# Kernel tuning notes

Measured on AMD Instinct MI355X. Metric: run time of the kernel, lower is better.

The kernel has to match this reference:

```python
import jax, jax.numpy as jnp
import numpy as np
from jax import lax

DH = 256   # d_hidden
NL = 8     # number of wavenet cells
K = 3      # kernel_size
DIN = 16   # d_lag + d_cov
DOUT = 1
T, B = 1024, 64


def setup_inputs() -> dict:
    key = jax.random.key(0)
    ks = jax.random.split(key, 20)
    s = 0.05
    inp = {
        "X_emb": jax.random.randint(ks[0], (T, B, 1), 0, 10),
        "X_cov": jax.random.normal(ks[1], (T, B, 8), jnp.float32),
        "X_lag": jax.random.normal(ks[2], (T, B, 8), jnp.float32),
        "y": jax.random.normal(ks[3], (T, B, DOUT), jnp.float32),
        "domain": jax.random.uniform(ks[4], (B, 4), jnp.float32),
        "up_w": jax.random.normal(ks[5], (DIN, DH), jnp.float32) * s,
        "up_b": jnp.zeros((DH,), jnp.float32),
        "conv_dil_w": jax.random.normal(ks[6], (NL, 2 * DH, DH, K), jnp.float32) * s,
        "conv_dil_b": jnp.zeros((NL, 2 * DH), jnp.float32),
        "skip_w": jax.random.normal(ks[7], (NL, 2 * DH, DH), jnp.float32) * s,
        "skip_b": jnp.zeros((NL, 2 * DH), jnp.float32),
        "fc_w": jax.random.normal(ks[8], (DH, DH), jnp.float32) * s,
        "fc_b": jnp.zeros((DH,), jnp.float32),
        "loc_w": jax.random.normal(ks[9], (DH, DOUT), jnp.float32) * s,
        "loc_b": jnp.zeros((DOUT,), jnp.float32),
        "scale_w": jax.random.normal(ks[10], (DH, DOUT), jnp.float32) * s,
        "scale_b": jnp.zeros((DOUT,), jnp.float32),
        "d_outputseqlen": 24,
    }
    return inp


def _causal_conv(h, w, b, dil):
    # h: [B, C, T], w: [O, C, K] -> causal (left-padded) dilated conv
    pad = (w.shape[-1] - 1) * dil
    y = lax.conv_general_dilated(h, w, window_strides=(1,), padding=[(pad, 0)],
                                 rhs_dilation=(dil,),
                                 dimension_numbers=("NCH", "OIH", "NCH"))
    return y + b[None, :, None]


def _forward(X_cov, X_lag, y, up_w, up_b, conv_dil_w, conv_dil_b,
             skip_w, skip_b, fc_w, fc_b, loc_w, loc_b, scale_w, scale_b,
             d_outputseqlen):
    t = X_lag.shape[0]
    h = jnp.concatenate([X_lag, X_cov[:t]], axis=-1) @ up_w + up_b  # [T,B,DH]
    h = jnp.transpose(h, (1, 2, 0))  # [B, DH, T]
    skip = jnp.zeros_like(h)
    for i in range(NL):
        fg = _causal_conv(h, conv_dil_w[i], conv_dil_b[i], 2 ** i)  # [B,2DH,T]
        f, g = jnp.split(fg, 2, axis=1)
        gated = jnp.tanh(f) * jax.nn.sigmoid(g)  # [B,DH,T]
        hs = jnp.einsum("oc,bct->bot", skip_w[i], gated) + skip_b[i][None, :, None]
        h_next, skip_next = jnp.split(hs, 2, axis=1)
        h = h + h_next
        skip = skip + skip_next
    feat = jnp.transpose(skip, (2, 0, 1))  # [T,B,DH]
    ff = jax.nn.relu(feat @ fc_w + fc_b)
    tail = ff[-d_outputseqlen:]
    loc = tail @ loc_w + loc_b
    scale = jax.nn.softplus(tail @ scale_w + scale_b) + 1e-6
    yt = y[-d_outputseqlen:]
    log_prob = (-0.5 * ((yt - loc) / scale) ** 2
                - jnp.log(scale) - 0.5 * np.log(2.0 * np.pi))
    loss_y = -jnp.mean(log_prob)
    total_loss = loss_y  # loss_d forced to 0 in the original forward
    return total_loss, loss_y, loc, scale


def reference(X_emb, X_cov, X_lag, y, domain, up_w, up_b, conv_dil_w,
              conv_dil_b, skip_w, skip_b, fc_w, fc_b, loc_w, loc_b,
              scale_w, scale_b, d_outputseqlen):
    # X_emb and domain are unused with d_emb=[] and loss_d hard-set to 0.
    return _forward(X_cov, X_lag, y, up_w, up_b, conv_dil_w, conv_dil_b,
                    skip_w, skip_b, fc_w, fc_b, loc_w, loc_b,
                    scale_w, scale_b, d_outputseqlen)
```

## Files before the change

kernel.cpp:

```cpp
#include <hip/hip_runtime.h>
#include <math.h>

static constexpr int TT = 1024, BB = 64, DHID = 256, NLAY = 8, OSL = 24;
static constexpr int T0H = 192, THN = 832;
static constexpr int T0G = 256, TGN = 768;

typedef __attribute__((ext_vector_type(8))) short short8;
typedef __attribute__((ext_vector_type(4))) float f32x4;
typedef unsigned short u16;
typedef __attribute__((ext_vector_type(4))) unsigned short u16x4;
typedef unsigned int u32;

__device__ __forceinline__ u16 f2bf(float x) {
  u32 u = __float_as_uint(x);
  return (u16)((u + 0x7fffu + ((u >> 16) & 1u)) >> 16);
}
__device__ __forceinline__ float bf2f(u16 v) {
  return __uint_as_float((u32)v << 16);
}
__device__ __forceinline__ void gll16(const u16* g, u16* l) {
  __builtin_amdgcn_global_load_lds((const __attribute__((address_space(1))) void*)g,
                                   (__attribute__((address_space(3))) void*)l, 16, 0, 0);
}

__global__ __launch_bounds__(256) void wprep(
    const float* __restrict__ cw, const float* __restrict__ sw,
    u16* __restrict__ wP, u16* __restrict__ swH, u16* __restrict__ swG)
{
  const int stride = gridDim.x * 256;
  for (int i = blockIdx.x * 256 + threadIdx.x; i < NLAY * 3 * 8 * 2 * 4 * 2048; i += stride) {
    const int e = i & 7, row = (i >> 3) & 255;
    int q = i >> 11;
    const int p = q & 3; q >>= 2;
    const int cs = q & 1; q >>= 1;
    const int kc = q & 7; q >>= 3;
    const int tap = q % 3, l = q / 3;
    const int o = (row < 128) ? (cs * 128 + row) : (256 + cs * 128 + (row - 128));
    const int c = kc * 32 + p * 8 + e;
    wP[i] = f2bf(cw[((size_t)(l * 512 + o) * 256 + c) * 3 + tap]);
  }
  for (int i = blockIdx.x * 256 + threadIdx.x; i < NLAY * 8 * 4 * 2048; i += stride) {
    const int e = i & 7, o = (i >> 3) & 255, p = (i >> 11) & 3, kc = (i >> 13) & 7, l = i >> 16;
    const int c = kc * 32 + p * 8 + e;
    swH[i] = f2bf(sw[(size_t)(l * 512 + o) * 256 + c]);
    swG[i] = f2bf(sw[(size_t)(l * 512 + 256 + o) * 256 + c]);
  }
}

__global__ __launch_bounds__(256) void up_kernel(
    const float* __restrict__ xlag, const float* __restrict__ xcov,
    const float* __restrict__ upw, const float* __restrict__ upb,
    u16* __restrict__ hb0)
{
  const int b  = blockIdx.y;
  const int t0 = T0H + blockIdx.x * 16;
  __shared__ float xs[16][17];
  {
    const int tl = threadIdx.x >> 4;
    const int j  = threadIdx.x & 15;
    const size_t base = ((size_t)(t0 + tl) * BB + b) * 8;
    xs[tl][j] = (j < 8) ? xlag[base + j] : xcov[base + (j - 8)];
  }
  __syncthreads();
  const int c = threadIdx.x;
  float uw[16];
#pragma unroll
  for (int j = 0; j < 16; ++j) uw[j] = upw[j * DHID + c];
  const float bias = upb[c];
#pragma unroll
  for (int tl = 0; tl < 16; ++tl) {
    float acc = bias;
#pragma unroll
    for (int j = 0; j < 16; ++j) acc = fmaf(xs[tl][j], uw[j], acc);
    hb0[(((size_t)b * 32 + (c >> 3)) * THN + (t0 + tl - T0H)) * 8 + (c & 7)] = f2bf(acc);
  }
}

__global__ __launch_bounds__(1024) void conv_gate(
    const u16* __restrict__ hbin, const u16* __restrict__ wPl,
    const float* __restrict__ cb, u16* __restrict__ gbuf,
    u16* __restrict__ g15l, const int dil, const int tile0)
{
  __shared__ u16 AB[2][16384];
  const int tid = threadIdx.x, w = tid >> 6, lane = tid & 63;
  const int l16 = lane & 15, quad = lane >> 4;
  const int mw = w & 3, nw = w >> 2;
  const int tile = tile0 + (int)(blockIdx.x >> 4);
  const int b0 = (blockIdx.x & 15) * 4;
  const int cs = blockIdx.y;
  const int t0 = tile * 64;

  f32x4 acc[4][4];
  const f32x4 zero = {0.f, 0.f, 0.f, 0.f};
#pragma unroll
  for (int m = 0; m < 4; ++m)
#pragma unroll
    for (int j = 0; j < 4; ++j) acc[m][j] = zero;

  const int ctb = tid >> 8, pb = (tid >> 6) & 3, tlb = tid & 63;

  auto stage = [&](int buf, int tap, int kc) {
    gll16(wPl + (size_t)(((tap * 8 + kc) * 2 + cs)) * 8192 + tid * 8,
          &AB[buf][(tid & ~63) * 8]);
    const int sh = (2 - tap) * dil;
    gll16(hbin + (((size_t)(b0 + ctb) * 32 + kc * 4 + pb) * THN + (t0 - sh - T0H + tlb)) * 8,
          &AB[buf][8192 + (tid & ~63) * 8]);
  };

  stage(0, 0, 0);
  __syncthreads();
  for (int step = 0; step < 24; ++step) {
    const int ns = step + 1;
    if (ns < 24) stage(ns & 1, ns >> 3, ns & 7);
    const u16* A = AB[step & 1];
    const u16* B = AB[step & 1] + 8192;
    short8 bfr[4];
#pragma unroll
    for (int j = 0; j < 4; ++j)
      bfr[j] = *(const short8*)&B[(nw * 256 + quad * 64 + 16 * j + l16) * 8];
#pragma unroll
    for (int m = 0; m < 4; ++m) {
      const int rowbase = (m < 2) ? (mw * 32 + 16 * m) : (128 + mw * 32 + 16 * (m - 2));
      const short8 a = *(const short8*)&A[(quad * 256 + rowbase + l16) * 8];
#pragma unroll
      for (int j = 0; j < 4; ++j)
        acc[m][j] = __builtin_amdgcn_mfma_f32_16x16x32_bf16(a, bfr[j], acc[m][j], 0, 0, 0);
    }
    __syncthreads();
  }

  u16* gT = (u16*)AB;
#pragma unroll
  for (int m = 0; m < 2; ++m) {
    const int c4 = mw * 32 + 16 * m + quad * 4;
    const int cpl = c4 >> 3;
#pragma unroll
    for (int j = 0; j < 4; ++j) {
      const int tl = 16 * j + l16;
      u16x4 pk;
#pragma unroll
      for (int r = 0; r < 4; ++r) {
        const float f = acc[m][j][r]     + cb[cs * 128 + c4 + r];
        const float g = acc[m + 2][j][r] + cb[256 + cs * 128 + c4 + r];
        const float th = 2.f / (1.f + __expf(-2.f * f)) - 1.f;
        const float sg = 1.f / (1.f + __expf(-g));
        pk[r] = f2bf(th * sg);
      }
      *(u16x4*)&gT[((nw * 16 + cpl) * 64 + tl) * 8 + (quad & 1) * 4] = pk;
    }
  }
  __syncthreads();
#pragma unroll
  for (int k = 0; k < 4; ++k) {
    const int slot = k * 1024 + tid;
    const int ct = slot >> 10, cpl = (slot >> 6) & 15, tl = slot & 63;
    const short8 v = *(const short8*)&gT[slot * 8];
    const int b = b0 + ct, cpg = cs * 16 + cpl;
    *(short8*)&gbuf[(((size_t)b * 32 + cpg) * TGN + (t0 + tl - T0G)) * 8] = v;
    if (tile == 15)
      *(short8*)&g15l[(((size_t)b * 32 + cpg) * 64 + tl) * 8] = v;
  }
}

__global__ __launch_bounds__(1024) void skip_h(
    const u16* __restrict__ gbuf, const u16* __restrict__ swHl,
    const float* __restrict__ sb, const u16* __restrict__ hbin,
    u16* __restrict__ hbout, const int tile0)
{
  __shared__ u16 AB[2][16384];
  const int tid = threadIdx.x, w = tid >> 6, lane = tid & 63;
  const int l16 = lane & 15, quad = lane >> 4;
  const int mw = w & 3, nw = w >> 2;
  const int tile = tile0 + (int)(blockIdx.x >> 4);
  const int b0 = (blockIdx.x & 15) * 4;
  const int t0 = tile * 64;

  f32x4 acc[4][4];
  const f32x4 zero = {0.f, 0.f, 0.f, 0.f};
#pragma unroll
  for (int m = 0; m < 4; ++m)
#pragma unroll
    for (int j = 0; j < 4; ++j) acc[m][j] = zero;

  const int ctb = tid >> 8, pb = (tid >> 6) & 3, tlb = tid & 63;

  auto stage = [&](int buf, int kc) {
    gll16(swHl + (size_t)kc * 8192 + tid * 8, &AB[buf][(tid & ~63) * 8]);
    gll16(gbuf + (((size_t)(b0 + ctb) * 32 + kc * 4 + pb) * TGN + (t0 - T0G + tlb)) * 8,
          &AB[buf][8192 + (tid & ~63) * 8]);
  };

  stage(0, 0);
  __syncthreads();
  for (int step = 0; step < 8; ++step) {
    if (step + 1 < 8) stage((step + 1) & 1, step + 1);
    const u16* A = AB[step & 1];
    const u16* B = AB[step & 1] + 8192;
    short8 bfr[4];
#pragma unroll
    for (int j = 0; j < 4; ++j)
      bfr[j] = *(const short8*)&B[(nw * 256 + quad * 64 + 16 * j + l16) * 8];
#pragma unroll
    for (int m = 0; m < 4; ++m) {
      const short8 a = *(const short8*)&A[(quad * 256 + mw * 64 + 16 * m + l16) * 8];
#pragma unroll
      for (int j = 0; j < 4; ++j)
        acc[m][j] = __builtin_amdgcn_mfma_f32_16x16x32_bf16(a, bfr[j], acc[m][j], 0, 0, 0);
    }
    __syncthreads();
  }

  float* fT = (float*)AB;
  for (int ctr = 0; ctr < 4; ++ctr) {
    __syncthreads();
    if (nw == ctr) {
#pragma unroll
      for (int m = 0; m < 4; ++m) {
        const int c4 = mw * 64 + 16 * m + quad * 4;
#pragma unroll
        for (int j = 0; j < 4; ++j) {
          const int tl = 16 * j + l16;
          f32x4 v;
#pragma unroll
          for (int r = 0; r < 4; ++r) v[r] = acc[m][j][r] + sb[c4 + r];
          *(f32x4*)&fT[((c4 >> 3) * 64 + tl) * 8 + (quad & 1) * 4] = v;
        }
      }
    }
    __syncthreads();
    const int b = b0 + ctr;
#pragma unroll
    for (int k = 0; k < 2; ++k) {
      const int slot = k * 1024 + tid;
      const int cpl = slot >> 6, tl = slot & 63;
      const size_t idx = (((size_t)b * 32 + cpl) * THN + (t0 - T0H + tl)) * 8;
      const short8 hv = *(const short8*)&hbin[idx];
      short8 ov;
#pragma unroll
      for (int e = 0; e < 8; ++e)
        ov[e] = (short)f2bf(bf2f((u16)hv[e]) + fT[slot * 8 + e]);
      *(short8*)&hbout[idx] = ov;
    }
  }
}

__global__ __launch_bounds__(1024) void skip_g_final(
    const u16* __restrict__ g15, const u16* __restrict__ swG,
    float* __restrict__ skipf)
{
  __shared__ u16 AB[2][10240];
  const int tid = threadIdx.x, w = tid >> 6, lane = tid & 63;
  const int l16 = lane & 15, quad = lane >> 4;
  const int b = blockIdx.x;

  f32x4 acc[4];
  const f32x4 zero = {0.f, 0.f, 0.f, 0.f};
#pragma unroll
  for (int j = 0; j < 4; ++j) acc[j] = zero;

  auto stage = [&](int buf, int ks) {
    gll16(swG + (size_t)ks * 8192 + tid * 8, &AB[buf][(tid & ~63) * 8]);
    if (tid < 256) {
      const int p = tid >> 6, tl = tid & 63;
      const int l = ks >> 3, kc = ks & 7;
      gll16(g15 + ((((size_t)l * 64 + b) * 32 + kc * 4 + p) * 64 + tl) * 8,
            &AB[buf][8192 + (tid & ~63) * 8]);
    }
  };

  stage(0, 0);
  __syncthreads();
  for (int step = 0; step < 64; ++step) {
    if (step + 1 < 64) stage((step + 1) & 1, step + 1);
    const u16* A = AB[step & 1];
    const u16* B = AB[step & 1] + 8192;
    const short8 a = *(const short8*)&A[(quad * 256 + w * 16 + l16) * 8];
#pragma unroll
    for (int j = 0; j < 4; ++j) {
      const short8 bf = *(const short8*)&B[(quad * 64 + 16 * j + l16) * 8];
      acc[j] = __builtin_amdgcn_mfma_f32_16x16x32_bf16(a, bf, acc[j], 0, 0, 0);
    }
    __syncthreads();
  }
#pragma unroll
  for (int j = 0; j < 4; ++j)
#pragma unroll
    for (int r = 0; r < 4; ++r) {
      const int c = w * 16 + quad * 4 + r;
      skipf[((size_t)b * 256 + c) * 64 + 16 * j + l16] = acc[j][r];
    }
}

__global__ __launch_bounds__(256) void head_kernel(
    const float* __restrict__ skipf, const float* __restrict__ skip_b,
    const float* __restrict__ fcw, const float* __restrict__ fcb,
    const float* __restrict__ locw, const float* __restrict__ locb,
    const float* __restrict__ scw, const float* __restrict__ scb,
    float* __restrict__ out)
{
  const int tt = blockIdx.x;
  const int b  = blockIdx.y;
  const int tl = 40 + tt;
  const int c  = threadIdx.x;
  __shared__ float xs[DHID];
  float sbg = 0.f;
#pragma unroll
  for (int l = 0; l < NLAY; ++l) sbg += skip_b[l * 512 + 256 + c];
  xs[c] = skipf[((size_t)b * 256 + c) * 64 + tl] + sbg;
  __syncthreads();
  float acc = fcb[c];
#pragma unroll 8
  for (int j = 0; j < DHID; ++j) acc = fmaf(xs[j], fcw[j * DHID + c], acc);
  const float ff = fmaxf(acc, 0.f);
  float pl = ff * locw[c];
  float ps = ff * scw[c];
#pragma unroll
  for (int off = 32; off > 0; off >>= 1) {
    pl += __shfl_down(pl, off);
    ps += __shfl_down(ps, off);
  }
  __shared__ float rl[4], rs[4];
  const int wid = threadIdx.x >> 6, lane = threadIdx.x & 63;
  if (lane == 0) { rl[wid] = pl; rs[wid] = ps; }
  __syncthreads();
  if (threadIdx.x == 0) {
    const float loc = rl[0] + rl[1] + rl[2] + rl[3] + locb[0];
    const float x   = rs[0] + rs[1] + rs[2] + rs[3] + scb[0];
    const float sp  = (x > 0.f) ? (x + log1pf(expf(-x))) : log1pf(expf(x));
    out[2 + tt * BB + b]            = loc;
    out[2 + OSL * BB + tt * BB + b] = sp + 1e-6f;
  }
}

__global__ __launch_bounds__(256) void loss_kernel(
    const float* __restrict__ y, float* __restrict__ out)
{
  float s = 0.f;
  for (int i = threadIdx.x; i < OSL * BB; i += 256) {
    const int tt = i >> 6, b = i & 63;
    const float loc = out[2 + i];
    const float sc  = out[2 + OSL * BB + i];
    const float yt  = y[(size_t)(TT - OSL + tt) * BB + b];
    const float z   = (yt - loc) / sc;
    s += -0.5f * z * z - logf(sc) - 0.9189385332046727f;
  }
#pragma unroll
  for (int off = 32; off > 0; off >>= 1) s += __shfl_down(s, off);
  __shared__ float r[4];
  if ((threadIdx.x & 63) == 0) r[threadIdx.x >> 6] = s;
  __syncthreads();
  if (threadIdx.x == 0) {
    const float loss = -(r[0] + r[1] + r[2] + r[3]) / (float)(OSL * BB);
    out[0] = loss;
    out[1] = loss;
  }
}

extern "C" void kernel_launch(void* const* d_in, const int* in_sizes, int n_in,
                              void* d_out, int out_size, void* d_ws, size_t ws_size,
                              hipStream_t stream) {
  (void)in_sizes; (void)n_in; (void)out_size; (void)ws_size;
  const float* X_cov  = (const float*)d_in[1];
  const float* X_lag  = (const float*)d_in[2];
  const float* y      = (const float*)d_in[3];
  const float* up_w   = (const float*)d_in[5];
  const float* up_b   = (const float*)d_in[6];
  const float* conv_w = (const float*)d_in[7];
  const float* conv_b = (const float*)d_in[8];
  const float* skip_w = (const float*)d_in[9];
  const float* skip_b = (const float*)d_in[10];
  const float* fc_w   = (const float*)d_in[11];
  const float* fc_b   = (const float*)d_in[12];
  const float* loc_w  = (const float*)d_in[13];
  const float* loc_b  = (const float*)d_in[14];
  const float* sc_w   = (const float*)d_in[15];
  const float* sc_b   = (const float*)d_in[16];

  char* wsb = (char*)d_ws;
  u16*   hb0   = (u16*)(wsb + 0);
  u16*   hb1   = (u16*)(wsb + 27262976);
  u16*   gbuf  = (u16*)(wsb + 54525952);
  u16*   g15   = (u16*)(wsb + 79691776);
  u16*   wP    = (u16*)(wsb + 96468992);
  u16*   swH   = (u16*)(wsb + 102760448);
  u16*   swG   = (u16*)(wsb + 103809024);
  float* skipf = (float*)(wsb + 104857600);

  wprep<<<1024, 256, 0, stream>>>(conv_w, skip_w, wP, swH, swG);
  up_kernel<<<dim3(52, BB), 256, 0, stream>>>(X_lag, X_cov, up_w, up_b, hb0);

  static const int Ptab[NLAY] = {4, 5, 6, 7, 8, 9, 11, 15};
  u16* hin = hb0;
  u16* hout = hb1;
  for (int i = 0; i < NLAY; ++i) {
    const int ntiles = 16 - Ptab[i];
    conv_gate<<<dim3(ntiles * 16, 2), 1024, 0, stream>>>(
        hin, wP + (size_t)i * 393216, conv_b + i * 512, gbuf,
        g15 + (size_t)i * 1048576, 1 << i, Ptab[i]);
    skip_h<<<dim3(ntiles * 16), 1024, 0, stream>>>(
        gbuf, swH + (size_t)i * 65536, skip_b + i * 512, hin, hout, Ptab[i]);
    u16* tmp = hin; hin = hout; hout = tmp;
  }

  skip_g_final<<<dim3(64), 1024, 0, stream>>>(g15, swG, skipf);
  head_kernel<<<dim3(OSL, BB), 256, 0, stream>>>(
      skipf, skip_b, fc_w, fc_b, loc_w, loc_b, sc_w, sc_b, (float*)d_out);
  loss_kernel<<<1, 256, 0, stream>>>(y, (float*)d_out);
}
```

Measured before the change: 665.8 us.

## Halve block sizes, split output channels finer, and parallelize final skip GEMM by layer

conv_gate now uses 512-thread blocks covering 64 output channels each, with four channel splits instead of two, and the weight prepack layout changes to match. skip_h uses 512-thread blocks over two batch entries each, doubling the grid. The serial 64-step final skip GEMM becomes a per-layer grid over only the needed 32 time steps, and the head sums the per-layer partials. The aim is more blocks and better occupancy on a machine with many CUs, at the cost of more redundant activation loads per block and extra partial-sum traffic.

```diff
diff --git a/kernel.cpp b/kernel.cpp
--- a/kernel.cpp
+++ b/kernel.cpp
@@ -28,14 +28,12 @@
     u16* __restrict__ wP, u16* __restrict__ swH, u16* __restrict__ swG)
 {
   const int stride = gridDim.x * 256;
-  for (int i = blockIdx.x * 256 + threadIdx.x; i < NLAY * 3 * 8 * 2 * 4 * 2048; i += stride) {
-    const int e = i & 7, row = (i >> 3) & 255;
-    int q = i >> 11;
-    const int p = q & 3; q >>= 2;
-    const int cs = q & 1; q >>= 1;
-    const int kc = q & 7; q >>= 3;
+  for (int i = blockIdx.x * 256 + threadIdx.x; i < NLAY * 3 * 8 * 4 * 4 * 128 * 8; i += stride) {
+    const int e = i & 7, row = (i >> 3) & 127;
+    const int p = (i >> 10) & 3, cs = (i >> 12) & 3, kc = (i >> 14) & 7;
+    const int q = i >> 17;
     const int tap = q % 3, l = q / 3;
-    const int o = (row < 128) ? (cs * 128 + row) : (256 + cs * 128 + (row - 128));
+    const int o = (row < 64) ? (cs * 64 + row) : (256 + cs * 64 + (row - 64));
     const int c = kc * 32 + p * 8 + e;
     wP[i] = f2bf(cw[((size_t)(l * 512 + o) * 256 + c) * 3 + tap]);
   }
@@ -76,15 +74,15 @@
   }
 }
 
-__global__ __launch_bounds__(1024) void conv_gate(
+__global__ __launch_bounds__(512, 6) void conv_gate(
     const u16* __restrict__ hbin, const u16* __restrict__ wPl,
     const float* __restrict__ cb, u16* __restrict__ gbuf,
     u16* __restrict__ g15l, const int dil, const int tile0)
 {
-  __shared__ u16 AB[2][16384];
+  __shared__ u16 AB[2][12288];
   const int tid = threadIdx.x, w = tid >> 6, lane = tid & 63;
   const int l16 = lane & 15, quad = lane >> 4;
-  const int mw = w & 3, nw = w >> 2;
+  const int mw = w & 1, nw = w >> 1;
   const int tile = tile0 + (int)(blockIdx.x >> 4);
   const int b0 = (blockIdx.x & 15) * 4;
   const int cs = blockIdx.y;
@@ -97,14 +95,17 @@
 #pragma unroll
     for (int j = 0; j < 4; ++j) acc[m][j] = zero;
 
-  const int ctb = tid >> 8, pb = (tid >> 6) & 3, tlb = tid & 63;
-
   auto stage = [&](int buf, int tap, int kc) {
-    gll16(wPl + (size_t)(((tap * 8 + kc) * 2 + cs)) * 8192 + tid * 8,
+    gll16(wPl + ((size_t)((tap * 8 + kc) * 4 + cs)) * 4096 + tid * 8,
           &AB[buf][(tid & ~63) * 8]);
     const int sh = (2 - tap) * dil;
-    gll16(hbin + (((size_t)(b0 + ctb) * 32 + kc * 4 + pb) * THN + (t0 - sh - T0H + tlb)) * 8,
-          &AB[buf][8192 + (tid & ~63) * 8]);
+#pragma unroll
+    for (int q = 0; q < 2; ++q) {
+      const int s = q * 512 + tid;
+      const int ct = s >> 8, p = (s >> 6) & 3, tl = s & 63;
+      gll16(hbin + (((size_t)(b0 + ct) * 32 + kc * 4 + p) * THN + (t0 - sh - T0H + tl)) * 8,
+            &AB[buf][4096 + (s & ~63) * 8]);
+    }
   };
 
   stage(0, 0, 0);
@@ -113,15 +114,15 @@
     const int ns = step + 1;
     if (ns < 24) stage(ns & 1, ns >> 3, ns & 7);
     const u16* A = AB[step & 1];
-    const u16* B = AB[step & 1] + 8192;
+    const u16* B = AB[step & 1] + 4096;
     short8 bfr[4];
 #pragma unroll
     for (int j = 0; j < 4; ++j)
       bfr[j] = *(const short8*)&B[(nw * 256 + quad * 64 + 16 * j + l16) * 8];
 #pragma unroll
     for (int m = 0; m < 4; ++m) {
-      const int rowbase = (m < 2) ? (mw * 32 + 16 * m) : (128 + mw * 32 + 16 * (m - 2));
-      const short8 a = *(const short8*)&A[(quad * 256 + rowbase + l16) * 8];
+      const int row = (m < 2) ? (mw * 32 + 16 * m) : (64 + mw * 32 + 16 * (m - 2));
+      const short8 a = *(const short8*)&A[(quad * 128 + row + l16) * 8];
 #pragma unroll
       for (int j = 0; j < 4; ++j)
         acc[m][j] = __builtin_amdgcn_mfma_f32_16x16x32_bf16(a, bfr[j], acc[m][j], 0, 0, 0);
@@ -133,46 +134,45 @@
 #pragma unroll
   for (int m = 0; m < 2; ++m) {
     const int c4 = mw * 32 + 16 * m + quad * 4;
-    const int cpl = c4 >> 3;
 #pragma unroll
     for (int j = 0; j < 4; ++j) {
       const int tl = 16 * j + l16;
       u16x4 pk;
 #pragma unroll
       for (int r = 0; r < 4; ++r) {
-        const float f = acc[m][j][r]     + cb[cs * 128 + c4 + r];
-        const float g = acc[m + 2][j][r] + cb[256 + cs * 128 + c4 + r];
+        const float f = acc[m][j][r]     + cb[cs * 64 + c4 + r];
+        const float g = acc[m + 2][j][r] + cb[256 + cs * 64 + c4 + r];
         const float th = 2.f / (1.f + __expf(-2.f * f)) - 1.f;
         const float sg = 1.f / (1.f + __expf(-g));
         pk[r] = f2bf(th * sg);
       }
-      *(u16x4*)&gT[((nw * 16 + cpl) * 64 + tl) * 8 + (quad & 1) * 4] = pk;
+      *(u16x4*)&gT[((nw * 8 + (c4 >> 3)) * 64 + tl) * 8 + (c4 & 7)] = pk;
     }
   }
   __syncthreads();
 #pragma unroll
   for (int k = 0; k < 4; ++k) {
-    const int slot = k * 1024 + tid;
-    const int ct = slot >> 10, cpl = (slot >> 6) & 15, tl = slot & 63;
+    const int slot = k * 512 + tid;
+    const int ct = slot >> 9, cpl = (slot >> 6) & 7, tl = slot & 63;
     const short8 v = *(const short8*)&gT[slot * 8];
-    const int b = b0 + ct, cpg = cs * 16 + cpl;
+    const int b = b0 + ct, cpg = cs * 8 + cpl;
     *(short8*)&gbuf[(((size_t)b * 32 + cpg) * TGN + (t0 + tl - T0G)) * 8] = v;
     if (tile == 15)
       *(short8*)&g15l[(((size_t)b * 32 + cpg) * 64 + tl) * 8] = v;
   }
 }
 
-__global__ __launch_bounds__(1024) void skip_h(
+__global__ __launch_bounds__(512, 6) void skip_h(
     const u16* __restrict__ gbuf, const u16* __restrict__ swHl,
     const float* __restrict__ sb, const u16* __restrict__ hbin,
     u16* __restrict__ hbout, const int tile0)
 {
-  __shared__ u16 AB[2][16384];
+  __shared__ u16 AB[2][12288];
   const int tid = threadIdx.x, w = tid >> 6, lane = tid & 63;
   const int l16 = lane & 15, quad = lane >> 4;
   const int mw = w & 3, nw = w >> 2;
-  const int tile = tile0 + (int)(blockIdx.x >> 4);
-  const int b0 = (blockIdx.x & 15) * 4;
+  const int tile = tile0 + (int)(blockIdx.x >> 5);
+  const int b0 = (blockIdx.x & 31) * 2;
   const int t0 = tile * 64;
 
   f32x4 acc[4][4];
@@ -182,11 +182,14 @@
 #pragma unroll
     for (int j = 0; j < 4; ++j) acc[m][j] = zero;
 
-  const int ctb = tid >> 8, pb = (tid >> 6) & 3, tlb = tid & 63;
-
   auto stage = [&](int buf, int kc) {
-    gll16(swHl + (size_t)kc * 8192 + tid * 8, &AB[buf][(tid & ~63) * 8]);
-    gll16(gbuf + (((size_t)(b0 + ctb) * 32 + kc * 4 + pb) * TGN + (t0 - T0G + tlb)) * 8,
+#pragma unroll
+    for (int q = 0; q < 2; ++q) {
+      const int s = q * 512 + tid;
+      gll16(swHl + (size_t)kc * 8192 + s * 8, &AB[buf][(s & ~63) * 8]);
+    }
+    const int ct = tid >> 8, p = (tid >> 6) & 3, tl = tid & 63;
+    gll16(gbuf + (((size_t)(b0 + ct) * 32 + kc * 4 + p) * TGN + (t0 - T0G + tl)) * 8,
           &AB[buf][8192 + (tid & ~63) * 8]);
   };
 
@@ -211,88 +214,103 @@
   }
 
   float* fT = (float*)AB;
-  for (int ctr = 0; ctr < 4; ++ctr) {
-    __syncthreads();
-    if (nw == ctr) {
-#pragma unroll
-      for (int m = 0; m < 4; ++m) {
-        const int c4 = mw * 64 + 16 * m + quad * 4;
-#pragma unroll
-        for (int j = 0; j < 4; ++j) {
-          const int tl = 16 * j + l16;
-          f32x4 v;
-#pragma unroll
-          for (int r = 0; r < 4; ++r) v[r] = acc[m][j][r] + sb[c4 + r];
-          *(f32x4*)&fT[((c4 >> 3) * 64 + tl) * 8 + (quad & 1) * 4] = v;
+  for (int ctr = 0; ctr < 2; ++ctr) {
+    for (int hh = 0; hh < 2; ++hh) {
+      __syncthreads();
+      if (nw == ctr && (mw >> 1) == hh) {
+#pragma unroll
+        for (int m = 0; m < 4; ++m) {
+          const int c4 = mw * 64 + 16 * m + quad * 4;
+          const int rl = c4 & 127;
+#pragma unroll
+          for (int j = 0; j < 4; ++j) {
+            const int tl = 16 * j + l16;
+            f32x4 v;
+#pragma unroll
+            for (int r = 0; r < 4; ++r) v[r] = acc[m][j][r] + sb[c4 + r];
+            *(f32x4*)&fT[((rl >> 3) * 64 + tl) * 8 + (rl & 7)] = v;
+          }
         }
       }
-    }
-    __syncthreads();
-    const int b = b0 + ctr;
-#pragma unroll
-    for (int k = 0; k < 2; ++k) {
-      const int slot = k * 1024 + tid;
-      const int cpl = slot >> 6, tl = slot & 63;
-      const size_t idx = (((size_t)b * 32 + cpl) * THN + (t0 - T0H + tl)) * 8;
-      const short8 hv = *(const short8*)&hbin[idx];
-      short8 ov;
-#pragma unroll
-      for (int e = 0; e < 8; ++e)
-        ov[e] = (short)f2bf(bf2f((u16)hv[e]) + fT[slot * 8 + e]);
-      *(short8*)&hbout[idx] = ov;
-    }
-  }
-}
-
-__global__ __launch_bounds__(1024) void skip_g_final(
+      __syncthreads();
+      const int b = b0 + ctr;
+#pragma unroll
+      for (int k = 0; k < 2; ++k) {
+        const int slot = k * 512 + tid;
+        const int cpl = slot >> 6, tl = slot & 63;
+        const size_t idx = (((size_t)b * 32 + hh * 16 + cpl) * THN + (t0 - T0H + tl)) * 8;
+        const short8 hv = *(const short8*)&hbin[idx];
+        short8 ov;
+#pragma unroll
+        for (int e = 0; e < 8; ++e)
+          ov[e] = (short)f2bf(bf2f((u16)hv[e]) + fT[slot * 8 + e]);
+        *(short8*)&hbout[idx] = ov;
+      }
+    }
+  }
+}
+
+__global__ __launch_bounds__(512) void skip_g(
     const u16* __restrict__ g15, const u16* __restrict__ swG,
-    float* __restrict__ skipf)
-{
-  __shared__ u16 AB[2][10240];
+    float* __restrict__ gpart)
+{
+  __shared__ u16 AB[2][9216];
   const int tid = threadIdx.x, w = tid >> 6, lane = tid & 63;
   const int l16 = lane & 15, quad = lane >> 4;
-  const int b = blockIdx.x;
-
-  f32x4 acc[4];
+  const int b = blockIdx.x, l = blockIdx.y;
+
+  f32x4 acc[2][2];
   const f32x4 zero = {0.f, 0.f, 0.f, 0.f};
 #pragma unroll
-  for (int j = 0; j < 4; ++j) acc[j] = zero;
-
-  auto stage = [&](int buf, int ks) {
-    gll16(swG + (size_t)ks * 8192 + tid * 8, &AB[buf][(tid & ~63) * 8]);
-    if (tid < 256) {
-      const int p = tid >> 6, tl = tid & 63;
-      const int l = ks >> 3, kc = ks & 7;
-      gll16(g15 + ((((size_t)l * 64 + b) * 32 + kc * 4 + p) * 64 + tl) * 8,
+  for (int m = 0; m < 2; ++m)
+#pragma unroll
+    for (int j = 0; j < 2; ++j) acc[m][j] = zero;
+
+  auto stage = [&](int buf, int kc) {
+#pragma unroll
+    for (int q = 0; q < 2; ++q) {
+      const int s = q * 512 + tid;
+      gll16(swG + ((size_t)l * 8 + kc) * 8192 + s * 8, &AB[buf][(s & ~63) * 8]);
+    }
+    if (tid < 128) {
+      const int p = tid >> 5, tl = tid & 31;
+      gll16(g15 + ((((size_t)l * 64 + b) * 32 + kc * 4 + p) * 64 + 32 + tl) * 8,
             &AB[buf][8192 + (tid & ~63) * 8]);
     }
   };
 
   stage(0, 0);
   __syncthreads();
-  for (int step = 0; step < 64; ++step) {
-    if (step + 1 < 64) stage((step + 1) & 1, step + 1);
+  for (int step = 0; step < 8; ++step) {
+    if (step + 1 < 8) stage((step + 1) & 1, step + 1);
     const u16* A = AB[step & 1];
     const u16* B = AB[step & 1] + 8192;
-    const short8 a = *(const short8*)&A[(quad * 256 + w * 16 + l16) * 8];
-#pragma unroll
-    for (int j = 0; j < 4; ++j) {
-      const short8 bf = *(const short8*)&B[(quad * 64 + 16 * j + l16) * 8];
-      acc[j] = __builtin_amdgcn_mfma_f32_16x16x32_bf16(a, bf, acc[j], 0, 0, 0);
+    short8 bfr[2];
+#pragma unroll
+    for (int j = 0; j < 2; ++j)
+      bfr[j] = *(const short8*)&B[(quad * 32 + 16 * j + l16) * 8];
+#pragma unroll
+    for (int m = 0; m < 2; ++m) {
+      const short8 a = *(const short8*)&A[(quad * 256 + w * 32 + 16 * m + l16) * 8];
+#pragma unroll
+      for (int j = 0; j < 2; ++j)
+        acc[m][j] = __builtin_amdgcn_mfma_f32_16x16x32_bf16(a, bfr[j], acc[m][j], 0, 0, 0);
     }
     __syncthreads();
   }
 #pragma unroll
-  for (int j = 0; j < 4; ++j)
-#pragma unroll
-    for (int r = 0; r < 4; ++r) {
-      const int c = w * 16 + quad * 4 + r;
-      skipf[((size_t)b * 256 + c) * 64 + 16 * j + l16] = acc[j][r];
-    }
+  for (int m = 0; m < 2; ++m)
+#pragma unroll
+    for (int j = 0; j < 2; ++j)
+#pragma unroll
+      for (int r = 0; r < 4; ++r) {
+        const int c = w * 32 + 16 * m + quad * 4 + r;
+        gpart[(((size_t)l * 64 + b) * 256 + c) * 32 + 16 * j + l16] = acc[m][j][r];
+      }
 }
 
 __global__ __launch_bounds__(256) void head_kernel(
-    const float* __restrict__ skipf, const float* __restrict__ skip_b,
+    const float* __restrict__ gpart, const float* __restrict__ skip_b,
     const float* __restrict__ fcw, const float* __restrict__ fcb,
     const float* __restrict__ locw, const float* __restrict__ locb,
     const float* __restrict__ scw, const float* __restrict__ scb,
@@ -300,13 +318,15 @@
 {
   const int tt = blockIdx.x;
   const int b  = blockIdx.y;
-  const int tl = 40 + tt;
   const int c  = threadIdx.x;
   __shared__ float xs[DHID];
-  float sbg = 0.f;
-#pragma unroll
-  for (int l = 0; l < NLAY; ++l) sbg += skip_b[l * 512 + 256 + c];
-  xs[c] = skipf[((size_t)b * 256 + c) * 64 + tl] + sbg;
+  float s = 0.f;
+#pragma unroll
+  for (int l = 0; l < NLAY; ++l) {
+    s += skip_b[l * 512 + 256 + c];
+    s += gpart[(((size_t)l * 64 + b) * 256 + c) * 32 + (8 + tt)];
+  }
+  xs[c] = s;
   __syncthreads();
   float acc = fcb[c];
 #pragma unroll 8
@@ -384,7 +404,7 @@
   u16*   wP    = (u16*)(wsb + 96468992);
   u16*   swH   = (u16*)(wsb + 102760448);
   u16*   swG   = (u16*)(wsb + 103809024);
-  float* skipf = (float*)(wsb + 104857600);
+  float* gpart = (float*)(wsb + 104857600);
 
   wprep<<<1024, 256, 0, stream>>>(conv_w, skip_w, wP, swH, swG);
   up_kernel<<<dim3(52, BB), 256, 0, stream>>>(X_lag, X_cov, up_w, up_b, hb0);
@@ -394,16 +414,16 @@
   u16* hout = hb1;
   for (int i = 0; i < NLAY; ++i) {
     const int ntiles = 16 - Ptab[i];
-    conv_gate<<<dim3(ntiles * 16, 2), 1024, 0, stream>>>(
+    conv_gate<<<dim3(ntiles * 16, 4), 512, 0, stream>>>(
         hin, wP + (size_t)i * 393216, conv_b + i * 512, gbuf,
         g15 + (size_t)i * 1048576, 1 << i, Ptab[i]);
-    skip_h<<<dim3(ntiles * 16), 1024, 0, stream>>>(
+    skip_h<<<dim3(ntiles * 32), 512, 0, stream>>>(
         gbuf, swH + (size_t)i * 65536, skip_b + i * 512, hin, hout, Ptab[i]);
     u16* tmp = hin; hin = hout; hout = tmp;
   }
 
-  skip_g_final<<<dim3(64), 1024, 0, stream>>>(g15, swG, skipf);
+  skip_g<<<dim3(64, 8), 512, 0, stream>>>(g15, swG, gpart);
   head_kernel<<<dim3(OSL, BB), 256, 0, stream>>>(
-      skipf, skip_b, fc_w, fc_b, loc_w, loc_b, sc_w, sc_b, (float*)d_out);
+      gpart, skip_b, fc_w, fc_b, loc_w, loc_b, sc_w, sc_b, (float*)d_out);
   loss_kernel<<<1, 256, 0, stream>>>(y, (float*)d_out);
 }
```

Result: slower. 1.484 ms (+122.8%).

## Replace LDS-direct loads with register-staged prefetch and split skip_g across layers

Applied to the files above, without the earlier changes.

In conv_gate and skip_h, global_load_lds DMA is replaced by loading the next tile into registers, running the MFMAs, then writing the registers to LDS before the barrier. The aim is to hide global latency behind compute. Separately, the serial 64-step skip_g_final is split into a 64x8 grid, one block per batch and layer, computing only the 32 needed timesteps. Per-layer partials are written out and summed in head_kernel. This adds parallelism at the cost of more register pressure and extra partial-sum traffic.

```diff
diff --git a/kernel.cpp b/kernel.cpp
--- a/kernel.cpp
+++ b/kernel.cpp
@@ -17,10 +17,6 @@
 }
 __device__ __forceinline__ float bf2f(u16 v) {
   return __uint_as_float((u32)v << 16);
-}
-__device__ __forceinline__ void gll16(const u16* g, u16* l) {
-  __builtin_amdgcn_global_load_lds((const __attribute__((address_space(1))) void*)g,
-                                   (__attribute__((address_space(3))) void*)l, 16, 0, 0);
 }
 
 __global__ __launch_bounds__(256) void wprep(
@@ -90,6 +86,17 @@
   const int cs = blockIdx.y;
   const int t0 = tile * 64;
 
+  const int ctb = tid >> 8, pb = (tid >> 6) & 3, tlb = tid & 63;
+
+  auto loadA = [&](int tap, int kc) -> short8 {
+    return *(const short8*)(wPl + ((size_t)((tap * 8 + kc) * 2 + cs)) * 8192 + tid * 8);
+  };
+  auto loadB = [&](int tap, int kc) -> short8 {
+    const int sh = (2 - tap) * dil;
+    return *(const short8*)(hbin +
+        (((size_t)(b0 + ctb) * 32 + kc * 4 + pb) * THN + (t0 - sh - T0H + tlb)) * 8);
+  };
+
   f32x4 acc[4][4];
   const f32x4 zero = {0.f, 0.f, 0.f, 0.f};
 #pragma unroll
@@ -97,21 +104,21 @@
 #pragma unroll
     for (int j = 0; j < 4; ++j) acc[m][j] = zero;
 
-  const int ctb = tid >> 8, pb = (tid >> 6) & 3, tlb = tid & 63;
-
-  auto stage = [&](int buf, int tap, int kc) {
-    gll16(wPl + (size_t)(((tap * 8 + kc) * 2 + cs)) * 8192 + tid * 8,
-          &AB[buf][(tid & ~63) * 8]);
-    const int sh = (2 - tap) * dil;
-    gll16(hbin + (((size_t)(b0 + ctb) * 32 + kc * 4 + pb) * THN + (t0 - sh - T0H + tlb)) * 8,
-          &AB[buf][8192 + (tid & ~63) * 8]);
-  };
-
-  stage(0, 0, 0);
-  __syncthreads();
+  {
+    short8 va = loadA(0, 0);
+    short8 vb = loadB(0, 0);
+    *(short8*)&AB[0][(size_t)tid * 8] = va;
+    *(short8*)&AB[0][8192 + (size_t)tid * 8] = vb;
+  }
+  __syncthreads();
+
   for (int step = 0; step < 24; ++step) {
     const int ns = step + 1;
-    if (ns < 24) stage(ns & 1, ns >> 3, ns & 7);
+    short8 va, vb;
+    if (ns < 24) {
+      va = loadA(ns >> 3, ns & 7);
+      vb = loadB(ns >> 3, ns & 7);
+    }
     const u16* A = AB[step & 1];
     const u16* B = AB[step & 1] + 8192;
     short8 bfr[4];
@@ -120,11 +127,15 @@
       bfr[j] = *(const short8*)&B[(nw * 256 + quad * 64 + 16 * j + l16) * 8];
 #pragma unroll
     for (int m = 0; m < 4; ++m) {
-      const int rowbase = (m < 2) ? (mw * 32 + 16 * m) : (128 + mw * 32 + 16 * (m - 2));
-      const short8 a = *(const short8*)&A[(quad * 256 + rowbase + l16) * 8];
+      const int row = (m < 2) ? (mw * 32 + 16 * m) : (128 + mw * 32 + 16 * (m - 2));
+      const short8 a = *(const short8*)&A[(quad * 256 + row + l16) * 8];
 #pragma unroll
       for (int j = 0; j < 4; ++j)
         acc[m][j] = __builtin_amdgcn_mfma_f32_16x16x32_bf16(a, bfr[j], acc[m][j], 0, 0, 0);
+    }
+    if (ns < 24) {
+      *(short8*)&AB[ns & 1][(size_t)tid * 8] = va;
+      *(short8*)&AB[ns & 1][8192 + (size_t)tid * 8] = vb;
     }
     __syncthreads();
   }
@@ -175,6 +186,16 @@
   const int b0 = (blockIdx.x & 15) * 4;
   const int t0 = tile * 64;
 
+  const int ctb = tid >> 8, pb = (tid >> 6) & 3, tlb = tid & 63;
+
+  auto loadA = [&](int kc) -> short8 {
+    return *(const short8*)(swHl + (size_t)kc * 8192 + tid * 8);
+  };
+  auto loadB = [&](int kc) -> short8 {
+    return *(const short8*)(gbuf +
+        (((size_t)(b0 + ctb) * 32 + kc * 4 + pb) * TGN + (t0 - T0G + tlb)) * 8);
+  };
+
   f32x4 acc[4][4];
   const f32x4 zero = {0.f, 0.f, 0.f, 0.f};
 #pragma unroll
@@ -182,18 +203,18 @@
 #pragma unroll
     for (int j = 0; j < 4; ++j) acc[m][j] = zero;
 
-  const int ctb = tid >> 8, pb = (tid >> 6) & 3, tlb = tid & 63;
-
-  auto stage = [&](int buf, int kc) {
-    gll16(swHl + (size_t)kc * 8192 + tid * 8, &AB[buf][(tid & ~63) * 8]);
-    gll16(gbuf + (((size_t)(b0 + ctb) * 32 + kc * 4 + pb) * TGN + (t0 - T0G + tlb)) * 8,
-          &AB[buf][8192 + (tid & ~63) * 8]);
-  };
-
-  stage(0, 0);
-  __syncthreads();
+  {
+    short8 va = loadA(0);
+    short8 vb = loadB(0);
+    *(short8*)&AB[0][(size_t)tid * 8] = va;
+    *(short8*)&AB[0][8192 + (size_t)tid * 8] = vb;
+  }
+  __syncthreads();
+
   for (int step = 0; step < 8; ++step) {
-    if (step + 1 < 8) stage((step + 1) & 1, step + 1);
+    const int ns = step + 1;
+    short8 va, vb;
+    if (ns < 8) { va = loadA(ns); vb = loadB(ns); }
     const u16* A = AB[step & 1];
     const u16* B = AB[step & 1] + 8192;
     short8 bfr[4];
@@ -206,6 +227,10 @@
 #pragma unroll
       for (int j = 0; j < 4; ++j)
         acc[m][j] = __builtin_amdgcn_mfma_f32_16x16x32_bf16(a, bfr[j], acc[m][j], 0, 0, 0);
+    }
+    if (ns < 8) {
+      *(short8*)&AB[ns & 1][(size_t)tid * 8] = va;
+      *(short8*)&AB[ns & 1][8192 + (size_t)tid * 8] = vb;
     }
     __syncthreads();
   }
@@ -244,55 +269,82 @@
   }
 }
 
-__global__ __launch_bounds__(1024) void skip_g_final(
+__global__ __launch_bounds__(512) void skip_g(
     const u16* __restrict__ g15, const u16* __restrict__ swG,
-    float* __restrict__ skipf)
-{
-  __shared__ u16 AB[2][10240];
+    float* __restrict__ gpart)
+{
+  __shared__ u16 AB[2][9216];
   const int tid = threadIdx.x, w = tid >> 6, lane = tid & 63;
   const int l16 = lane & 15, quad = lane >> 4;
-  const int b = blockIdx.x;
-
-  f32x4 acc[4];
+  const int b = blockIdx.x, l = blockIdx.y;
+
+  auto loadA = [&](int kc, int q) -> short8 {
+    return *(const short8*)(swG + ((size_t)l * 8 + kc) * 8192 + (q * 512 + tid) * 8);
+  };
+  auto loadB = [&](int kc) -> short8 {
+    const int p = tid >> 5, tl = tid & 31;
+    return *(const short8*)(g15 +
+        ((((size_t)l * 64 + b) * 32 + kc * 4 + p) * 64 + 32 + tl) * 8);
+  };
+
+  f32x4 acc[2][2];
   const f32x4 zero = {0.f, 0.f, 0.f, 0.f};
 #pragma unroll
-  for (int j = 0; j < 4; ++j) acc[j] = zero;
-
-  auto stage = [&](int buf, int ks) {
-    gll16(swG + (size_t)ks * 8192 + tid * 8, &AB[buf][(tid & ~63) * 8]);
-    if (tid < 256) {
-      const int p = tid >> 6, tl = tid & 63;
-      const int l = ks >> 3, kc = ks & 7;
-      gll16(g15 + ((((size_t)l * 64 + b) * 32 + kc * 4 + p) * 64 + tl) * 8,
-            &AB[buf][8192 + (tid & ~63) * 8]);
-    }
-  };
-
-  stage(0, 0);
-  __syncthreads();
-  for (int step = 0; step < 64; ++step) {
-    if (step + 1 < 64) stage((step + 1) & 1, step + 1);
+  for (int m = 0; m < 2; ++m)
+#pragma unroll
+    for (int j = 0; j < 2; ++j) acc[m][j] = zero;
+
+  {
+    short8 a0 = loadA(0, 0), a1 = loadA(0, 1);
+    *(short8*)&AB[0][(size_t)tid * 8] = a0;
+    *(short8*)&AB[0][(size_t)(512 + tid) * 8] = a1;
+    if (tid < 128) {
+      short8 vb = loadB(0);
+      *(short8*)&AB[0][8192 + (size_t)tid * 8] = vb;
+    }
+  }
+  __syncthreads();
+
+  for (int step = 0; step < 8; ++step) {
+    const int ns = step + 1;
+    short8 a0, a1, vb;
+    if (ns < 8) {
+      a0 = loadA(ns, 0); a1 = loadA(ns, 1);
+      if (tid < 128) vb = loadB(ns);
+    }
     const u16* A = AB[step & 1];
     const u16* B = AB[step & 1] + 8192;
-    const short8 a = *(const short8*)&A[(quad * 256 + w * 16 + l16) * 8];
-#pragma unroll
-    for (int j = 0; j < 4; ++j) {
-      const short8 bf = *(const short8*)&B[(quad * 64 + 16 * j + l16) * 8];
-      acc[j] = __builtin_amdgcn_mfma_f32_16x16x32_bf16(a, bf, acc[j], 0, 0, 0);
+    short8 bfr[2];
+#pragma unroll
+    for (int j = 0; j < 2; ++j)
+      bfr[j] = *(const short8*)&B[(quad * 32 + 16 * j + l16) * 8];
+#pragma unroll
+    for (int m = 0; m < 2; ++m) {
+      const short8 a = *(const short8*)&A[(quad * 256 + w * 32 + 16 * m + l16) * 8];
+#pragma unroll
+      for (int j = 0; j < 2; ++j)
+        acc[m][j] = __builtin_amdgcn_mfma_f32_16x16x32_bf16(a, bfr[j], acc[m][j], 0, 0, 0);
+    }
+    if (ns < 8) {
+      *(short8*)&AB[ns & 1][(size_t)tid * 8] = a0;
+      *(short8*)&AB[ns & 1][(size_t)(512 + tid) * 8] = a1;
+      if (tid < 128) *(short8*)&AB[ns & 1][8192 + (size_t)tid * 8] = vb;
     }
     __syncthreads();
   }
 #pragma unroll
-  for (int j = 0; j < 4; ++j)
-#pragma unroll
-    for (int r = 0; r < 4; ++r) {
-      const int c = w * 16 + quad * 4 + r;
-      skipf[((size_t)b * 256 + c) * 64 + 16 * j + l16] = acc[j][r];
-    }
+  for (int m = 0; m < 2; ++m)
+#pragma unroll
+    for (int j = 0; j < 2; ++j)
+#pragma unroll
+      for (int r = 0; r < 4; ++r) {
+        const int c = w * 32 + 16 * m + quad * 4 + r;
+        gpart[(((size_t)l * 64 + b) * 256 + c) * 32 + 16 * j + l16] = acc[m][j][r];
+      }
 }
 
 __global__ __launch_bounds__(256) void head_kernel(
-    const float* __restrict__ skipf, const float* __restrict__ skip_b,
+    const float* __restrict__ gpart, const float* __restrict__ skip_b,
     const float* __restrict__ fcw, const float* __restrict__ fcb,
     const float* __restrict__ locw, const float* __restrict__ locb,
     const float* __restrict__ scw, const float* __restrict__ scb,
@@ -300,13 +352,15 @@
 {
   const int tt = blockIdx.x;
   const int b  = blockIdx.y;
-  const int tl = 40 + tt;
   const int c  = threadIdx.x;
   __shared__ float xs[DHID];
-  float sbg = 0.f;
-#pragma unroll
-  for (int l = 0; l < NLAY; ++l) sbg += skip_b[l * 512 + 256 + c];
-  xs[c] = skipf[((size_t)b * 256 + c) * 64 + tl] + sbg;
+  float s = 0.f;
+#pragma unroll
+  for (int l = 0; l < NLAY; ++l) {
+    s += skip_b[l * 512 + 256 + c];
+    s += gpart[(((size_t)l * 64 + b) * 256 + c) * 32 + (8 + tt)];
+  }
+  xs[c] = s;
   __syncthreads();
   float acc = fcb[c];
 #pragma unroll 8
@@ -384,7 +438,7 @@
   u16*   wP    = (u16*)(wsb + 96468992);
   u16*   swH   = (u16*)(wsb + 102760448);
   u16*   swG   = (u16*)(wsb + 103809024);
-  float* skipf = (float*)(wsb + 104857600);
+  float* gpart = (float*)(wsb + 104857600);
 
   wprep<<<1024, 256, 0, stream>>>(conv_w, skip_w, wP, swH, swG);
   up_kernel<<<dim3(52, BB), 256, 0, stream>>>(X_lag, X_cov, up_w, up_b, hb0);
@@ -402,8 +456,8 @@
     u16* tmp = hin; hin = hout; hout = tmp;
   }
 
-  skip_g_final<<<dim3(64), 1024, 0, stream>>>(g15, swG, skipf);
+  skip_g<<<dim3(64, 8), 512, 0, stream>>>(g15, swG, gpart);
   head_kernel<<<dim3(OSL, BB), 256, 0, stream>>>(
-      skipf, skip_b, fc_w, fc_b, loc_w, loc_b, sc_w, sc_b, (float*)d_out);
+      gpart, skip_b, fc_w, fc_b, loc_w, loc_b, sc_w, sc_b, (float*)d_out);
   loss_kernel<<<1, 256, 0, stream>>>(y, (float*)d_out);
 }
```

Measured after the change: 731.2 us. 1.1x slower.
